# Kernel tuning notes

Measured on AMD Instinct MI355X. Metric: run time of the kernel, lower is better.

Reference implementation:

```python
import jax, jax.numpy as jnp
import numpy as np

B, N, D = 8, 2048, 1024
DQ, DV = 1024, 1024


def setup_inputs() -> dict:
    key = jax.random.key(0)
    ks = jax.random.split(key, 7)
    s = 1.0 / np.sqrt(D)
    return {
        "x": jax.random.normal(ks[0], (B, N, D), dtype=jnp.float32),
        "Wq": jax.random.uniform(ks[1], (D, DQ), jnp.float32, -s, s),
        "bq": jax.random.uniform(ks[2], (DQ,), jnp.float32, -s, s),
        "Wk": jax.random.uniform(ks[3], (D, DQ), jnp.float32, -s, s),
        "bk": jax.random.uniform(ks[4], (DQ,), jnp.float32, -s, s),
        "Wv": jax.random.uniform(ks[5], (D, DV), jnp.float32, -s, s),
        "bv": jax.random.uniform(ks[6], (DV,), jnp.float32, -s, s),
    }


def reference(x, Wq, bq, Wk, bk, Wv, bv):
    # Linear projections (nn.Linear: x @ W + b)
    Q = jnp.einsum("bnd,dq->bnq", x, Wq) + bq  # [B,N,DQ]
    K = jnp.einsum("bnd,dq->bnq", x, Wk) + bk  # [B,N,DQ]
    V = jnp.einsum("bnd,dv->bnv", x, Wv) + bv  # [B,N,DV]
    # NOTE: original forward does NOT apply the 1/sqrt(dk) scaling.
    scores = jnp.einsum("bnq,bmq->bnm", Q, K)  # [B,N,N]
    attn = jax.nn.softmax(scores, axis=-1)
    out = jnp.einsum("bnm,bmv->bnv", attn, V)  # [B,N,DV]
    return out
```

## Files before the change

### kernel.cpp

```cpp
#include <hip/hip_runtime.h>
#include <hip/hip_bf16.h>
#include <stdint.h>


typedef _Float16 f16;
typedef _Float16 f16x8 __attribute__((ext_vector_type(8)));
typedef _Float16 f16x4 __attribute__((ext_vector_type(4)));
typedef float f32x4 __attribute__((ext_vector_type(4)));

typedef __attribute__((address_space(3))) void lds_void;
typedef const __attribute__((address_space(1))) void gbl_void;

__device__ __forceinline__ void async16(void* l, const void* g) {
    __builtin_amdgcn_global_load_lds(
        reinterpret_cast<gbl_void*>(reinterpret_cast<uintptr_t>(g)),
        reinterpret_cast<lds_void*>(reinterpret_cast<uintptr_t>(l)),
        16, 0, 0);
}

__global__ __launch_bounds__(256) void cast_f32_f16(const float* __restrict__ x,
                                                    f16* __restrict__ y) {
    long i = (long)blockIdx.x * 256 + threadIdx.x;
    float4 v = reinterpret_cast<const float4*>(x)[i];
    f16x4 o = {(f16)v.x, (f16)v.y, (f16)v.z, (f16)v.w};
    reinterpret_cast<f16x4*>(y)[i] = o;
}

__global__ __launch_bounds__(256) void transpose_cast3(const float* __restrict__ W0,
                                                       const float* __restrict__ W1,
                                                       const float* __restrict__ W2,
                                                       f16* __restrict__ wt) {
    const float* W = blockIdx.z == 0 ? W0 : blockIdx.z == 1 ? W1 : W2;
    f16* o = wt + (long)blockIdx.z * 1024 * 1024;
    __shared__ float tile[32][33];
    int c0 = blockIdx.x * 32, r0 = blockIdx.y * 32;
    int tx = threadIdx.x, ty = threadIdx.y;
#pragma unroll
    for (int i = ty; i < 32; i += 8) tile[i][tx] = W[(long)(r0 + i) * 1024 + c0 + tx];
    __syncthreads();
#pragma unroll
    for (int i = ty; i < 32; i += 8) o[(long)(c0 + i) * 1024 + r0 + tx] = (f16)tile[tx][i];
}

#define GEMM_CORE(A_, lda_, B_, ldb_, K_)                                         \
    f32x4 acc[4][4] = {};                                                         \
    const int sr = tid >> 3;                                                      \
    const int sj = tid & 7;                                                       \
    for (int k0 = 0; k0 < (K_); k0 += 64) {                                       \
        _Pragma("unroll") for (int i = 0; i < 4; ++i) {                           \
            int u = i * 256 + tid;                                                \
            int r = sr + i * 32;                                                  \
            int c = (sj ^ (r & 7)) * 8;                                           \
            async16((char*)As + u * 16, (A_) + (mBase + r) * (long)(lda_) + k0 + c); \
            async16((char*)Bs + u * 16, (B_) + (nBase + r) * (long)(ldb_) + k0 + c); \
        }                                                                         \
        __syncthreads();                                                          \
        _Pragma("unroll") for (int ks = 0; ks < 2; ++ks) {                        \
            f16x8 af[4], bfr[4];                                                  \
            const int q8 = (lane >> 4) * 8 + ks * 32;                             \
            const int ra = wm + (lane & 15);                                      \
            const int rb = wn + (lane & 15);                                      \
            const int cc = (((q8 >> 3) ^ (lane & 7)) << 3);                       \
            _Pragma("unroll") for (int t = 0; t < 4; ++t) {                       \
                af[t] = *reinterpret_cast<const f16x8*>(&As[(ra + t * 16) * 64 + cc]); \
                bfr[t] = *reinterpret_cast<const f16x8*>(&Bs[(rb + t * 16) * 64 + cc]); \
            }                                                                     \
            _Pragma("unroll") for (int am = 0; am < 4; ++am)                      \
                _Pragma("unroll") for (int an = 0; an < 4; ++an)                  \
                    acc[am][an] = __builtin_amdgcn_mfma_f32_16x16x32_f16(         \
                        af[am], bfr[an], acc[am][an], 0, 0, 0);                   \
        }                                                                         \
        __syncthreads();                                                          \
    }

#define GEMM_PRELUDE                                                              \
    __shared__ f16 As[128 * 64];                                                  \
    __shared__ f16 Bs[128 * 64];                                                  \
    const int tid = threadIdx.x;                                                  \
    const int lane = tid & 63;                                                    \
    const int wv = tid >> 6;                                                      \
    const int wm = (wv >> 1) * 64;                                                \
    const int wn = (wv & 1) * 64;

#define SUPER_DECODE(j_, MT_, my_, nx_)                                           \
    {                                                                             \
        int w_ = (j_) & 31, s_ = (j_) >> 5;                                       \
        int sm_ = s_ % ((MT_) / 8), sn_ = s_ / ((MT_) / 8);                       \
        my_ = sm_ * 8 + (w_ & 7);                                                 \
        nx_ = sn_ * 4 + (w_ >> 3);                                                \
    }

template <int DEC>
__global__ __launch_bounds__(256) void gemm_bt(
    const f16* __restrict__ A, long sA, int lda,
    const f16* __restrict__ Bt, long sB, int ldb,
    void* __restrict__ outv, long sO, int ldo, int K) {
    GEMM_PRELUDE
    const int L = blockIdx.x;
    const int xcd = L & 7, j = L >> 3;
    int by, bx;
    SUPER_DECODE(j, 16, by, bx)
    const long mBase = (long)by * 128;
    const long nBase = (long)bx * 128;
    A += (long)xcd * sA;
    Bt += (long)xcd * sB;

    GEMM_CORE(A, lda, Bt, ldb, K)

    const int rq = (lane >> 4) * 4;
    const int cl = lane & 15;
#pragma unroll
    for (int am = 0; am < 4; ++am)
#pragma unroll
        for (int an = 0; an < 4; ++an) {
            long col = nBase + wn + an * 16 + cl;
#pragma unroll
            for (int r = 0; r < 4; ++r) {
                long row = mBase + wm + am * 16 + rq + r;
                if (DEC == 1) {
                    ((f16*)outv)[(long)xcd * sO + row * ldo + col] = (f16)acc[am][an][r];
                } else {
                    ((float*)outv)[(long)xcd * sO + row * ldo + col] = acc[am][an][r];
                }
            }
        }
}

__global__ __launch_bounds__(256) void gemm_qkv(
    const f16* __restrict__ xh, const f16* __restrict__ wt,
    const float* __restrict__ bq, const float* __restrict__ bk,
    const float* __restrict__ bv,
    f16* __restrict__ Q, f16* __restrict__ Kb, f16* __restrict__ Vt) {
    GEMM_PRELUDE
    const int L = blockIdx.x;
    const int xcd = L & 7, j = L >> 3;
    int my, bx;
    SUPER_DECODE(j, 16, my, bx)
    const int by = xcd * 16 + my;
    const long mBase = (long)by * 128;
    const long nBase = (long)bx * 128;

    GEMM_CORE(xh, 1024, wt, 1024, 1024)

    const int seg = (int)(nBase >> 10);
    const float* bias = seg == 0 ? bq : seg == 1 ? bk : bv;
    f16* outQK = seg == 0 ? Q : Kb;
    const int rq = (lane >> 4) * 4;
    const int cl = lane & 15;
#pragma unroll
    for (int am = 0; am < 4; ++am)
#pragma unroll
        for (int an = 0; an < 4; ++an) {
            long col = nBase + wn + an * 16 + cl;
            long c = col & 1023;
            float bvv = bias[c];
#pragma unroll
            for (int r = 0; r < 4; ++r) {
                long row = mBase + wm + am * 16 + rq + r;
                float v = acc[am][an][r] + bvv;
                if (seg < 2) {
                    outQK[row * 1024 + c] = (f16)v;
                } else {
                    long bb = row >> 11, seq = row & 2047;
                    Vt[(bb * 1024 + c) * 2048 + seq] = (f16)v;
                }
            }
        }
}

__global__ __launch_bounds__(256) void softmax_rows(const f16* __restrict__ S,
                                                    f16* __restrict__ P) {
    const long row = blockIdx.x;
    const int t = threadIdx.x;
    f16x8 a = reinterpret_cast<const f16x8*>(S + row * 2048)[t];
    float e[8];
    float m = -1e30f;
#pragma unroll
    for (int j = 0; j < 8; ++j) { e[j] = (float)a[j]; m = fmaxf(m, e[j]); }
#pragma unroll
    for (int o = 32; o > 0; o >>= 1) m = fmaxf(m, __shfl_down(m, o, 64));
    __shared__ float red[8];
    if ((t & 63) == 0) red[t >> 6] = m;
    __syncthreads();
    m = fmaxf(fmaxf(red[0], red[1]), fmaxf(red[2], red[3]));
    float s = 0.0f;
#pragma unroll
    for (int j = 0; j < 8; ++j) { e[j] = __expf(e[j] - m); s += e[j]; }
#pragma unroll
    for (int o = 32; o > 0; o >>= 1) s += __shfl_down(s, o, 64);
    if ((t & 63) == 0) red[4 + (t >> 6)] = s;
    __syncthreads();
    s = red[4] + red[5] + red[6] + red[7];
    float inv = 1.0f / s;
    f16x8 o;
#pragma unroll
    for (int j = 0; j < 8; ++j) o[j] = (f16)(e[j] * inv);
    reinterpret_cast<f16x8*>(P + row * 2048)[t] = o;
}

extern "C" void kernel_launch(void* const* d_in, const int* in_sizes, int n_in,
                              void* d_out, int out_size, void* d_ws, size_t ws_size,
                              hipStream_t stream) {
    const float* x  = (const float*)d_in[0];
    const float* Wq = (const float*)d_in[1];
    const float* bq = (const float*)d_in[2];
    const float* Wk = (const float*)d_in[3];
    const float* bk = (const float*)d_in[4];
    const float* Wv = (const float*)d_in[5];
    const float* bv = (const float*)d_in[6];
    float* out = (float*)d_out;
    char* ws = (char*)d_ws;

    f16* Q   = (f16*)(ws + 0);
    f16* Kb  = (f16*)(ws + 33554432);
    f16* Vt  = (f16*)(ws + 67108864);
    f16* S16 = (f16*)(ws + 100663296);
    f16* P   = (f16*)(ws + 167772160);
    f16* xh  = (f16*)(ws + 100663296);
    f16* wt  = (f16*)(ws + 134217728);

    cast_f32_f16<<<16384, 256, 0, stream>>>(x, xh);
    transpose_cast3<<<dim3(32, 32, 3), dim3(32, 8), 0, stream>>>(Wq, Wk, Wv, wt);

    gemm_qkv<<<3072, 256, 0, stream>>>(xh, wt, bq, bk, bv, Q, Kb, Vt);

    gemm_bt<1><<<2048, 256, 0, stream>>>(Q, 2048L * 1024, 1024,
                                         Kb, 2048L * 1024, 1024,
                                         S16, 2048L * 2048, 2048, 1024);

    softmax_rows<<<16384, 256, 0, stream>>>(S16, P);

    gemm_bt<2><<<1024, 256, 0, stream>>>(P, 2048L * 2048, 2048,
                                         Vt, 1024L * 2048, 2048,
                                         out, 2048L * 1024, 1024, 2048);
}
```

Measured before the change: 474.1 us.

## Replace GEMM kernels with double-buffered 256x256 tile pipelined MFMA kernel

Replaces the three 128x128 single-buffered GEMMs with one templated 256x256-tile kernel using 512 threads and 128KB of double-buffered LDS. Asynchronous global-to-LDS loads for later k-steps are interleaved with MFMA phases, using explicit waitcnt, barriers and setprio to overlap memory with compute. Larger tiles raise arithmetic intensity and cut global traffic. In exchange, grids shrink to 768/512/256 blocks, which may underfill the CUs, especially the P·V GEMM, and the hand-written waitcnt counts are fragile.

```diff
diff --git a/kernel.cpp b/kernel.cpp
--- a/kernel.cpp
+++ b/kernel.cpp
@@ -42,130 +42,206 @@
     for (int i = ty; i < 32; i += 8) o[(long)(c0 + i) * 1024 + r0 + tx] = (f16)tile[tx][i];
 }
 
-#define GEMM_CORE(A_, lda_, B_, ldb_, K_)                                         \
-    f32x4 acc[4][4] = {};                                                         \
-    const int sr = tid >> 3;                                                      \
-    const int sj = tid & 7;                                                       \
-    for (int k0 = 0; k0 < (K_); k0 += 64) {                                       \
-        _Pragma("unroll") for (int i = 0; i < 4; ++i) {                           \
-            int u = i * 256 + tid;                                                \
-            int r = sr + i * 32;                                                  \
-            int c = (sj ^ (r & 7)) * 8;                                           \
-            async16((char*)As + u * 16, (A_) + (mBase + r) * (long)(lda_) + k0 + c); \
-            async16((char*)Bs + u * 16, (B_) + (nBase + r) * (long)(ldb_) + k0 + c); \
-        }                                                                         \
-        __syncthreads();                                                          \
-        _Pragma("unroll") for (int ks = 0; ks < 2; ++ks) {                        \
-            f16x8 af[4], bfr[4];                                                  \
-            const int q8 = (lane >> 4) * 8 + ks * 32;                             \
-            const int ra = wm + (lane & 15);                                      \
-            const int rb = wn + (lane & 15);                                      \
-            const int cc = (((q8 >> 3) ^ (lane & 7)) << 3);                       \
-            _Pragma("unroll") for (int t = 0; t < 4; ++t) {                       \
-                af[t] = *reinterpret_cast<const f16x8*>(&As[(ra + t * 16) * 64 + cc]); \
-                bfr[t] = *reinterpret_cast<const f16x8*>(&Bs[(rb + t * 16) * 64 + cc]); \
-            }                                                                     \
-            _Pragma("unroll") for (int am = 0; am < 4; ++am)                      \
-                _Pragma("unroll") for (int an = 0; an < 4; ++an)                  \
-                    acc[am][an] = __builtin_amdgcn_mfma_f32_16x16x32_f16(         \
-                        af[am], bfr[an], acc[am][an], 0, 0, 0);                   \
-        }                                                                         \
-        __syncthreads();                                                          \
+template <int MODE>
+__global__ __launch_bounds__(512, 2) void gemm256(
+    const f16* __restrict__ A, const f16* __restrict__ Bm,
+    f16* __restrict__ o16, float* __restrict__ o32,
+    const float* __restrict__ bq, const float* __restrict__ bk,
+    const float* __restrict__ bv,
+    f16* __restrict__ Qo, f16* __restrict__ Ko, f16* __restrict__ Vto) {
+    constexpr int LDA = MODE == 2 ? 2048 : 1024;
+    constexpr int LDB = MODE == 2 ? 2048 : 1024;
+    constexpr int NT = (MODE == 2 ? 2048 : 1024) / 64;
+
+    __shared__ f16 sm[65536];
+    char* smb = (char*)sm;
+
+    const int tid = threadIdx.x;
+    const int lane = tid & 63;
+    const int wv = tid >> 6;
+    const int wmi = wv >> 2;
+    const int wni = wv & 3;
+
+    const int L = blockIdx.x;
+    long mBase, nBase, oOff = 0;
+    int nx = 0;
+    if (MODE == 0) {
+        const int xcd = L & 7, j = L >> 3;
+        nx = j >> 3;
+        mBase = (long)(xcd * 8 + (j & 7)) * 256;
+        nBase = (long)nx * 256;
+    } else if (MODE == 1) {
+        const int b = L & 7, j = L >> 3;
+        mBase = (long)(j & 7) * 256;
+        nBase = (long)(j >> 3) * 256;
+        A += (long)b * 2048 * 1024;
+        Bm += (long)b * 2048 * 1024;
+        oOff = (long)b * 2048 * 2048;
+    } else {
+        const int b = L & 7, j = L >> 3;
+        mBase = (long)(j & 7) * 256;
+        nBase = (long)(j >> 3) * 256;
+        A += (long)b * 2048 * 2048;
+        Bm += (long)b * 1024 * 2048;
+        oOff = (long)b * 2048 * 1024;
     }
 
-#define GEMM_PRELUDE                                                              \
-    __shared__ f16 As[128 * 64];                                                  \
-    __shared__ f16 Bs[128 * 64];                                                  \
-    const int tid = threadIdx.x;                                                  \
-    const int lane = tid & 63;                                                    \
-    const int wv = tid >> 6;                                                      \
-    const int wm = (wv >> 1) * 64;                                                \
-    const int wn = (wv & 1) * 64;
-
-#define SUPER_DECODE(j_, MT_, my_, nx_)                                           \
-    {                                                                             \
-        int w_ = (j_) & 31, s_ = (j_) >> 5;                                       \
-        int sm_ = s_ % ((MT_) / 8), sn_ = s_ / ((MT_) / 8);                       \
-        my_ = sm_ * 8 + (w_ & 7);                                                 \
-        nx_ = sn_ * 4 + (w_ >> 3);                                                \
+    const int sru = tid >> 3;
+    const int sck = (tid & 7) ^ (sru & 7);
+    const f16* pA = A + (mBase + sru) * LDA + sck * 8;
+    const f16* pB = Bm + (nBase + sru) * LDB + sck * 8;
+
+    auto stA = [&](int bufB, int half, int t) {
+        const f16* s = pA + half * 128 * LDA + t * 64;
+        char* d = smb + bufB + half * 16384 + tid * 16;
+        async16(d, s);
+        async16(d + 8192, s + 64 * LDA);
+    };
+    auto stB = [&](int bufB, int half, int t) {
+        const f16* s = pB + half * 128 * LDB + t * 64;
+        char* d = smb + bufB + 32768 + half * 16384 + tid * 16;
+        async16(d, s);
+        async16(d + 8192, s + 64 * LDB);
+    };
+
+    const int pc0 = (lane >> 4) ^ (lane & 7);
+    const int aBase = (wmi * 128 + (lane & 15)) * 64 + pc0 * 8;
+    const int bBase = 16384 + (wni * 64 + (lane & 15)) * 64 + pc0 * 8;
+
+    stA(0, 0, 0); stA(0, 1, 0); stB(0, 0, 0); stB(0, 1, 0);
+    stA(65536, 0, 1); stA(65536, 1, 1); stB(65536, 0, 1);
+    asm volatile("s_waitcnt vmcnt(6)" ::: "memory");
+    __builtin_amdgcn_s_barrier();
+
+    f32x4 acc[8][4] = {};
+    for (int t = 0; t < NT; ++t) {
+        const int cE = (t & 1) << 15;
+        const int cB = (t & 1) << 16;
+        const int nB = cB ^ 65536;
+        f16x8 a0[8], a1[8], bA[2], bB[2], bC[2], bD[2];
+#pragma unroll
+        for (int mf = 0; mf < 8; ++mf)
+            a0[mf] = *reinterpret_cast<const f16x8*>(&sm[cE + aBase + mf * 1024]);
+#pragma unroll
+        for (int q = 0; q < 2; ++q)
+            bA[q] = *reinterpret_cast<const f16x8*>(&sm[cE + bBase + q * 1024]);
+#pragma unroll
+        for (int mf = 0; mf < 8; ++mf)
+            a1[mf] = *reinterpret_cast<const f16x8*>(&sm[cE + ((aBase + mf * 1024) ^ 32)]);
+        if (t + 1 < NT) stB(nB, 1, t + 1);
+        __builtin_amdgcn_s_barrier();
+        asm volatile("s_waitcnt lgkmcnt(8)" ::: "memory");
+        __builtin_amdgcn_sched_barrier(0);
+        __builtin_amdgcn_s_setprio(1);
+#pragma unroll
+        for (int mf = 0; mf < 8; ++mf) {
+            acc[mf][0] = __builtin_amdgcn_mfma_f32_16x16x32_f16(a0[mf], bA[0], acc[mf][0], 0, 0, 0);
+            acc[mf][1] = __builtin_amdgcn_mfma_f32_16x16x32_f16(a0[mf], bA[1], acc[mf][1], 0, 0, 0);
+        }
+        __builtin_amdgcn_s_setprio(0);
+        asm volatile("s_waitcnt lgkmcnt(0)" ::: "memory");
+        __builtin_amdgcn_s_barrier();
+#pragma unroll
+        for (int q = 0; q < 2; ++q)
+            bB[q] = *reinterpret_cast<const f16x8*>(&sm[cE + bBase + (2 + q) * 1024]);
+        if (t + 2 < NT) stA(cB, 0, t + 2);
+        __builtin_amdgcn_s_barrier();
+        asm volatile("s_waitcnt lgkmcnt(0)" ::: "memory");
+        __builtin_amdgcn_sched_barrier(0);
+        __builtin_amdgcn_s_setprio(1);
+#pragma unroll
+        for (int mf = 0; mf < 8; ++mf) {
+            acc[mf][2] = __builtin_amdgcn_mfma_f32_16x16x32_f16(a0[mf], bB[0], acc[mf][2], 0, 0, 0);
+            acc[mf][3] = __builtin_amdgcn_mfma_f32_16x16x32_f16(a0[mf], bB[1], acc[mf][3], 0, 0, 0);
+        }
+        __builtin_amdgcn_s_setprio(0);
+        __builtin_amdgcn_s_barrier();
+#pragma unroll
+        for (int q = 0; q < 2; ++q)
+            bC[q] = *reinterpret_cast<const f16x8*>(&sm[cE + ((bBase + q * 1024) ^ 32)]);
+#pragma unroll
+        for (int q = 0; q < 2; ++q)
+            bD[q] = *reinterpret_cast<const f16x8*>(&sm[cE + ((bBase + (2 + q) * 1024) ^ 32)]);
+        if (t + 2 < NT) stA(cB, 1, t + 2);
+        __builtin_amdgcn_s_barrier();
+        asm volatile("s_waitcnt lgkmcnt(2)" ::: "memory");
+        __builtin_amdgcn_sched_barrier(0);
+        __builtin_amdgcn_s_setprio(1);
+#pragma unroll
+        for (int mf = 0; mf < 8; ++mf) {
+            acc[mf][0] = __builtin_amdgcn_mfma_f32_16x16x32_f16(a1[mf], bC[0], acc[mf][0], 0, 0, 0);
+            acc[mf][1] = __builtin_amdgcn_mfma_f32_16x16x32_f16(a1[mf], bC[1], acc[mf][1], 0, 0, 0);
+        }
+        __builtin_amdgcn_s_setprio(0);
+        asm volatile("s_waitcnt lgkmcnt(0)" ::: "memory");
+        __builtin_amdgcn_s_barrier();
+        if (t + 2 < NT) stB(cB, 0, t + 2);
+        __builtin_amdgcn_s_barrier();
+        __builtin_amdgcn_s_setprio(1);
+#pragma unroll
+        for (int mf = 0; mf < 8; ++mf) {
+            acc[mf][2] = __builtin_amdgcn_mfma_f32_16x16x32_f16(a1[mf], bD[0], acc[mf][2], 0, 0, 0);
+            acc[mf][3] = __builtin_amdgcn_mfma_f32_16x16x32_f16(a1[mf], bD[1], acc[mf][3], 0, 0, 0);
+        }
+        __builtin_amdgcn_s_setprio(0);
+        if (t < NT - 2) {
+            asm volatile("s_waitcnt vmcnt(6)" ::: "memory");
+        } else {
+            asm volatile("s_waitcnt vmcnt(0)" ::: "memory");
+        }
+        __builtin_amdgcn_s_barrier();
     }
-
-template <int DEC>
-__global__ __launch_bounds__(256) void gemm_bt(
-    const f16* __restrict__ A, long sA, int lda,
-    const f16* __restrict__ Bt, long sB, int ldb,
-    void* __restrict__ outv, long sO, int ldo, int K) {
-    GEMM_PRELUDE
-    const int L = blockIdx.x;
-    const int xcd = L & 7, j = L >> 3;
-    int by, bx;
-    SUPER_DECODE(j, 16, by, bx)
-    const long mBase = (long)by * 128;
-    const long nBase = (long)bx * 128;
-    A += (long)xcd * sA;
-    Bt += (long)xcd * sB;
-
-    GEMM_CORE(A, lda, Bt, ldb, K)
 
     const int rq = (lane >> 4) * 4;
     const int cl = lane & 15;
-#pragma unroll
-    for (int am = 0; am < 4; ++am)
-#pragma unroll
-        for (int an = 0; an < 4; ++an) {
-            long col = nBase + wn + an * 16 + cl;
-#pragma unroll
-            for (int r = 0; r < 4; ++r) {
-                long row = mBase + wm + am * 16 + rq + r;
-                if (DEC == 1) {
-                    ((f16*)outv)[(long)xcd * sO + row * ldo + col] = (f16)acc[am][an][r];
-                } else {
-                    ((float*)outv)[(long)xcd * sO + row * ldo + col] = acc[am][an][r];
+    if (MODE == 0) {
+        const int seg = nx >> 2;
+        const float* bias = seg == 0 ? bq : seg == 1 ? bk : bv;
+        f16* outQK = seg == 0 ? Qo : Ko;
+#pragma unroll
+        for (int mf = 0; mf < 8; ++mf)
+#pragma unroll
+            for (int nf = 0; nf < 4; ++nf) {
+                const long c = (nBase & 1023) + wni * 64 + nf * 16 + cl;
+                const float bb = bias[c];
+#pragma unroll
+                for (int r = 0; r < 4; ++r) {
+                    const long row = mBase + wmi * 128 + mf * 16 + rq + r;
+                    const float v = acc[mf][nf][r] + bb;
+                    if (seg < 2) {
+                        outQK[row * 1024 + c] = (f16)v;
+                    } else {
+                        Vto[((row >> 11) * 1024 + c) * 2048 + (row & 2047)] = (f16)v;
+                    }
                 }
             }
-        }
-}
-
-__global__ __launch_bounds__(256) void gemm_qkv(
-    const f16* __restrict__ xh, const f16* __restrict__ wt,
-    const float* __restrict__ bq, const float* __restrict__ bk,
-    const float* __restrict__ bv,
-    f16* __restrict__ Q, f16* __restrict__ Kb, f16* __restrict__ Vt) {
-    GEMM_PRELUDE
-    const int L = blockIdx.x;
-    const int xcd = L & 7, j = L >> 3;
-    int my, bx;
-    SUPER_DECODE(j, 16, my, bx)
-    const int by = xcd * 16 + my;
-    const long mBase = (long)by * 128;
-    const long nBase = (long)bx * 128;
-
-    GEMM_CORE(xh, 1024, wt, 1024, 1024)
-
-    const int seg = (int)(nBase >> 10);
-    const float* bias = seg == 0 ? bq : seg == 1 ? bk : bv;
-    f16* outQK = seg == 0 ? Q : Kb;
-    const int rq = (lane >> 4) * 4;
-    const int cl = lane & 15;
-#pragma unroll
-    for (int am = 0; am < 4; ++am)
-#pragma unroll
-        for (int an = 0; an < 4; ++an) {
-            long col = nBase + wn + an * 16 + cl;
-            long c = col & 1023;
-            float bvv = bias[c];
-#pragma unroll
-            for (int r = 0; r < 4; ++r) {
-                long row = mBase + wm + am * 16 + rq + r;
-                float v = acc[am][an][r] + bvv;
-                if (seg < 2) {
-                    outQK[row * 1024 + c] = (f16)v;
-                } else {
-                    long bb = row >> 11, seq = row & 2047;
-                    Vt[(bb * 1024 + c) * 2048 + seq] = (f16)v;
+    } else if (MODE == 1) {
+        f16* o = o16 + oOff;
+#pragma unroll
+        for (int mf = 0; mf < 8; ++mf)
+#pragma unroll
+            for (int nf = 0; nf < 4; ++nf) {
+                const long col = nBase + wni * 64 + nf * 16 + cl;
+#pragma unroll
+                for (int r = 0; r < 4; ++r) {
+                    const long row = mBase + wmi * 128 + mf * 16 + rq + r;
+                    o[row * 2048 + col] = (f16)acc[mf][nf][r];
                 }
             }
-        }
+    } else {
+        float* o = o32 + oOff;
+#pragma unroll
+        for (int mf = 0; mf < 8; ++mf)
+#pragma unroll
+            for (int nf = 0; nf < 4; ++nf) {
+                const long col = nBase + wni * 64 + nf * 16 + cl;
+#pragma unroll
+                for (int r = 0; r < 4; ++r) {
+                    const long row = mBase + wmi * 128 + mf * 16 + rq + r;
+                    o[row * 1024 + col] = acc[mf][nf][r];
+                }
+            }
+    }
 }
 
 __global__ __launch_bounds__(256) void softmax_rows(const f16* __restrict__ S,
@@ -222,15 +298,16 @@
     cast_f32_f16<<<16384, 256, 0, stream>>>(x, xh);
     transpose_cast3<<<dim3(32, 32, 3), dim3(32, 8), 0, stream>>>(Wq, Wk, Wv, wt);
 
-    gemm_qkv<<<3072, 256, 0, stream>>>(xh, wt, bq, bk, bv, Q, Kb, Vt);
-
-    gemm_bt<1><<<2048, 256, 0, stream>>>(Q, 2048L * 1024, 1024,
-                                         Kb, 2048L * 1024, 1024,
-                                         S16, 2048L * 2048, 2048, 1024);
+    gemm256<0><<<768, 512, 0, stream>>>(xh, wt, nullptr, nullptr,
+                                        bq, bk, bv, Q, Kb, Vt);
+
+    gemm256<1><<<512, 512, 0, stream>>>(Q, Kb, S16, nullptr,
+                                        nullptr, nullptr, nullptr,
+                                        nullptr, nullptr, nullptr);
 
     softmax_rows<<<16384, 256, 0, stream>>>(S16, P);
 
-    gemm_bt<2><<<1024, 256, 0, stream>>>(P, 2048L * 2048, 2048,
-                                         Vt, 1024L * 2048, 2048,
-                                         out, 2048L * 1024, 1024, 2048);
-}
+    gemm256<2><<<256, 512, 0, stream>>>(P, Vt, nullptr, out,
+                                        nullptr, nullptr, nullptr,
+                                        nullptr, nullptr, nullptr);
+}
```

Result: faster. 402.0 us (-15.2%).
